# Kernel tuning notes

Hardware: AMD Instinct MI355X
Metric: run time of the kernel (lower is better)

The kernel has to match this reference:

```python
import jax, jax.numpy as jnp
import numpy as np

SCALE = 8.0  # sqrt(d_k=64)


def setup_inputs() -> dict:
    key = jax.random.key(0)
    kq, kk, kv, km = jax.random.split(key, 4)
    B, L, D = 8, 4096, 64
    q = jax.random.normal(kq, (B, L, D), dtype=jnp.float32)
    k = jax.random.normal(kk, (B, L, D), dtype=jnp.float32)
    v = jax.random.normal(kv, (B, L, D), dtype=jnp.float32)
    mask = jax.random.randint(km, (B, L, L), 0, 2) == 1  # True = masked out
    return {"q": q, "k": k, "v": v, "mask": mask}


def reference(q, k, v, mask):
    # scores: [B, Lq, Lk]
    u = jnp.einsum('bqd,bkd->bqk', q, k) / SCALE
    u = jnp.where(mask, -jnp.inf, u)
    attn = jax.nn.softmax(u, axis=2)
    output = jnp.einsum('bqk,bkd->bqd', attn, v)
    return (attn, output)
```

## Files before the change

### kernel.cpp

```cpp
#include <hip/hip_runtime.h>
#include <hip/hip_bf16.h>
#include <stdint.h>

#define BB 8
#define LL 4096
#define DD 64
#define KT 64
#define NT (LL / KT)
#define NP2 (LL / 128)

typedef short bf16x8 __attribute__((ext_vector_type(8)));
typedef float f32x4 __attribute__((ext_vector_type(4)));

#define QSCALE 0.1803368801111204f

__device__ inline short f2bfs(float x) {
    __hip_bfloat16 h = __float2bfloat16(x);
    return __builtin_bit_cast(short, h);
}

__device__ inline bf16x8 pack8v(f32x4 a, f32x4 b) {
    bf16x8 r;
    r[0] = f2bfs(a[0]); r[1] = f2bfs(a[1]); r[2] = f2bfs(a[2]); r[3] = f2bfs(a[3]);
    r[4] = f2bfs(b[0]); r[5] = f2bfs(b[1]); r[6] = f2bfs(b[2]); r[7] = f2bfs(b[3]);
    return r;
}

__device__ inline int swzK(int r) { return (r & 3) | (((r >> 3) & 1) << 2); }
__device__ inline int swzV(int r) { return (r & 7) ^ ((r >> 3) & 7); }

__device__ inline void wg_barrier() {
    asm volatile("s_waitcnt lgkmcnt(0)" ::: "memory");
    __builtin_amdgcn_s_barrier();
    __builtin_amdgcn_sched_barrier(0);
}

__device__ inline void gl_lds16(const ushort* g, ushort* l) {
    __builtin_amdgcn_global_load_lds((const __attribute__((address_space(1))) void*)g,
                                     (__attribute__((address_space(3))) void*)l, 16, 0, 0);
}

__global__ void detect_mask_kernel(const uint32_t* __restrict__ w, uint32_t* __restrict__ flag) {
    __shared__ int nonbin;
    if (threadIdx.x == 0) nonbin = 0;
    __syncthreads();
    int bad = 0;
    for (int i = threadIdx.x; i < 4096; i += 256) bad |= (w[i] > 1u) ? 1 : 0;
    if (bad) atomicOr(&nonbin, 1);
    __syncthreads();
    if (threadIdx.x == 0) *flag = (uint32_t)(nonbin != 0);
}

__global__ void convert_k_kernel(const float* __restrict__ src, ushort* __restrict__ dst) {
    const int i = blockIdx.x * 256 + threadIdx.x;
    f32x4 a = *(const f32x4*)(src + (size_t)i * 8);
    f32x4 b = *(const f32x4*)(src + (size_t)i * 8 + 4);
    *(bf16x8*)(dst + (size_t)i * 8) = pack8v(a, b);
}

__global__ void convert_vt_kernel(const float* __restrict__ v, ushort* __restrict__ vt) {
    __shared__ alignas(16) float Lt[64][68];
    const int kt = blockIdx.x, b = blockIdx.y;
    const int tid = (int)threadIdx.x;
    const int r = tid >> 2, c4 = tid & 3;
    const float* vb = v + ((size_t)b * LL + kt * 64) * DD;
    #pragma unroll
    for (int j = 0; j < 4; ++j)
        *(f32x4*)&Lt[r][c4 * 16 + j * 4] = *(const f32x4*)(vb + (size_t)r * DD + c4 * 16 + j * 4);
    __syncthreads();
    ushort* vout = vt + (size_t)b * DD * LL + (size_t)r * LL + kt * 64 + c4 * 16;
    bf16x8 o0, o1;
    #pragma unroll
    for (int j = 0; j < 8; ++j) o0[j] = f2bfs(Lt[c4 * 16 + j][r]);
    #pragma unroll
    for (int j = 0; j < 8; ++j) o1[j] = f2bfs(Lt[c4 * 16 + 8 + j][r]);
    *(bf16x8*)vout = o0;
    *(bf16x8*)(vout + 8) = o1;
}

__global__ __launch_bounds__(512, 4) void fused_attn_kernel(
    const float* __restrict__ qg, const ushort* __restrict__ kbf,
    const ushort* __restrict__ vtb, const void* __restrict__ maskv,
    const uint32_t* __restrict__ flagp,
    float* __restrict__ attn, float* __restrict__ outp)
{
    __shared__ alignas(16) ushort KB[4][KT * 64];
    __shared__ uint8_t Msk[8][NT][64];
    __shared__ float Rs[128];

    const int tid = (int)threadIdx.x;
    const int w   = tid >> 6, l = tid & 63;
    const int lr  = l & 15, lg = l >> 4;
    const int rg  = w & 3, ch = w >> 2;
    const int id  = (int)blockIdx.x;
    const int b   = id & 7;
    const int q0  = (id >> 3) * 64;
    const bool mbyte = (*flagp != 0);

    const ushort* kb = kbf + (size_t)b * LL * DD;
    const ushort* vtg = vtb + (size_t)b * DD * LL;

    const int qrow = q0 + 16 * rg + lr;
    const uint8_t* mrow8  = (const uint8_t*)maskv + (size_t)b * LL * LL + (size_t)qrow * LL + ch * 32 + lg * 8;
    const int*     mrow32 = (const int*)maskv     + (size_t)b * LL * LL + (size_t)qrow * LL + ch * 32 + lg * 8;
    float* arow = attn + (size_t)b * LL * LL + (size_t)qrow * LL + ch * 32 + lg * 8;

    bf16x8 qf0, qf1;
    {
        const float* qp = qg + (size_t)(b * LL + qrow) * DD + lg * 8;
        qf0 = pack8v(*(const f32x4*)(qp)      * QSCALE, *(const f32x4*)(qp + 4)  * QSCALE);
        qf1 = pack8v(*(const f32x4*)(qp + 32) * QSCALE, *(const f32x4*)(qp + 36) * QSCALE);
    }

    const int drow = w * 8 + (l >> 3);
    const int dc   = l & 7;
    const int kchunk = dc ^ swzK(drow);
    const int vchunk = dc ^ swzV(drow);
    auto dmaK = [&](int kt, int buf) {
        gl_lds16(kb + (size_t)(kt * KT + drow) * 64 + 8 * kchunk, &KB[buf][w * 512]);
    };
    auto dmaV = [&](int kt, int buf) {
        gl_lds16(vtg + (size_t)drow * LL + kt * KT + 8 * vchunk, &KB[2 + buf][w * 512]);
    };
    auto dmaK2 = [&](int kt2, int pair) {
        gl_lds16(kb + (size_t)(kt2 * 128 + drow) * 64 + 8 * kchunk, &KB[2 * pair][w * 512]);
        gl_lds16(kb + (size_t)(kt2 * 128 + 64 + drow) * 64 + 8 * kchunk, &KB[2 * pair + 1][w * 512]);
    };
    unsigned long long mA = 0, mB = 0;
    #define ASM_MLOAD(dst, kt) { unsigned long long a_ = (unsigned long long)(uintptr_t)(mrow8 + (kt) * KT); \
        asm volatile("global_load_dwordx2 %0, %1, off" : "=v"(dst) : "v"(a_) : "memory"); }

    float rsum = 0.f;
    f32x4 oacc[4];
    #pragma unroll
    for (int g = 0; g < 4; ++g) { f32x4 z = {0.f, 0.f, 0.f, 0.f}; oacc[g] = z; }

    auto body1 = [&](int buf, unsigned long long mu, int kt) {
        int4 mi0 = {0,0,0,0}, mi1 = {0,0,0,0};
        if (!mbyte) { mi0 = *(const int4*)(mrow32 + kt * KT); mi1 = *(const int4*)(mrow32 + kt * KT + 4); }
        uint32_t mbits = 0;
        float p8[8];
        __builtin_amdgcn_s_setprio(1);
        #pragma unroll
        for (int n = 0; n < 2; ++n) {
            const int krow = ch * 32 + ((lr >> 2) << 3) + (n << 2) + (lr & 3);
            bf16x8 k0 = *(const bf16x8*)&KB[buf][krow * 64 + ((lg       ^ swzK(krow)) << 3)];
            bf16x8 k1 = *(const bf16x8*)&KB[buf][krow * 64 + (((4 + lg) ^ swzK(krow)) << 3)];
            f32x4 c = {0.f, 0.f, 0.f, 0.f};
            c = __builtin_amdgcn_mfma_f32_16x16x32_bf16(k0, qf0, c, 0, 0, 0);
            c = __builtin_amdgcn_mfma_f32_16x16x32_bf16(k1, qf1, c, 0, 0, 0);
            #pragma unroll
            for (int j = 0; j < 4; ++j) {
                const int t = n * 4 + j;
                int mk;
                if (mbyte) mk = (int)((mu >> (8 * t)) & 0xffu);
                else {
                    const int4 mi = n ? mi1 : mi0;
                    mk = (j == 0) ? mi.x : (j == 1) ? mi.y : (j == 2) ? mi.z : mi.w;
                }
                mbits |= (mk ? 1u : 0u) << t;
                const float pv = mk ? 0.f : exp2f(c[j]);
                rsum += pv;
                p8[t] = pv;
            }
        }
        __builtin_amdgcn_s_setprio(0);
        Msk[w][kt][l] = (uint8_t)mbits;
        bf16x8 pa;
        #pragma unroll
        for (int t = 0; t < 8; ++t) pa[t] = f2bfs(p8[t]);
        __builtin_amdgcn_s_setprio(1);
        #pragma unroll
        for (int g = 0; g < 4; ++g) {
            const int d = g * 16 + lr;
            bf16x8 vf = *(const bf16x8*)&KB[2 + buf][d * 64 + (((ch * 4 + lg) ^ swzV(d)) << 3)];
            oacc[g] = __builtin_amdgcn_mfma_f32_16x16x32_bf16(pa, vf, oacc[g], 0, 0, 0);
        }
        __builtin_amdgcn_s_setprio(0);
    };

    dmaK(0, 0); dmaV(0, 0); if (mbyte) ASM_MLOAD(mA, 0);
    dmaK(1, 1); dmaV(1, 1); if (mbyte) ASM_MLOAD(mB, 1);
    #pragma unroll 1
    for (int kt = 0; kt < NT; kt += 2) {
        if (mbyte) asm volatile("s_waitcnt vmcnt(3)" ::: "memory");
        else       asm volatile("s_waitcnt vmcnt(2)" ::: "memory");
        __builtin_amdgcn_sched_barrier(0);
        wg_barrier();
        body1(0, mA, kt);
        wg_barrier();
        {
            const int nx = (kt + 2) & (NT - 1);
            dmaK(nx, 0); dmaV(nx, 0); if (mbyte) ASM_MLOAD(mA, nx);
        }
        if (mbyte) asm volatile("s_waitcnt vmcnt(3)" ::: "memory");
        else       asm volatile("s_waitcnt vmcnt(2)" ::: "memory");
        __builtin_amdgcn_sched_barrier(0);
        wg_barrier();
        body1(1, mB, kt + 1);
        wg_barrier();
        {
            const int nx = (kt + 3) & (NT - 1);
            dmaK(nx, 1); dmaV(nx, 1); if (mbyte) ASM_MLOAD(mB, nx);
        }
    }
    asm volatile("s_waitcnt vmcnt(0)" ::: "memory");

    rsum += __shfl_xor(rsum, 16, 64);
    rsum += __shfl_xor(rsum, 32, 64);
    if (lg == 0) Rs[ch * 64 + 16 * rg + lr] = rsum;
    __syncthreads();
    const float rinv = 1.0f / (Rs[16 * rg + lr] + Rs[64 + 16 * rg + lr]);

    float* OutL = (float*)KB;
    if (ch == 1) {
        #pragma unroll
        for (int g = 0; g < 4; ++g)
            #pragma unroll
            for (int j = 0; j < 4; ++j)
                OutL[rg * 1088 + (lg * 4 + j) * 68 + g * 16 + lr] = oacc[g][j];
    }
    __syncthreads();
    if (ch == 0) {
        #pragma unroll
        for (int j = 0; j < 4; ++j) {
            const int ql = 16 * rg + lg * 4 + j;
            const float ri = 1.0f / (Rs[ql] + Rs[64 + ql]);
            const size_t orow = (size_t)(b * LL + q0 + ql) * DD;
            #pragma unroll
            for (int g = 0; g < 4; ++g)
                outp[orow + g * 16 + lr] = (oacc[g][j] + OutL[rg * 1088 + (lg * 4 + j) * 68 + g * 16 + lr]) * ri;
        }
    }
    __syncthreads();

    auto body2 = [&](int pair, int idx) {
        const int kbase2 = idx * 128;
        #pragma unroll
        for (int h = 0; h < 2; ++h) {
            const int mb2 = (int)Msk[w][2 * idx + h][l];
            const ushort* Kbuf = KB[2 * pair + h];
            __builtin_amdgcn_s_setprio(1);
            #pragma unroll
            for (int n = 0; n < 2; ++n) {
                const int krow = ch * 32 + ((lr >> 2) << 3) + (n << 2) + (lr & 3);
                bf16x8 k0 = *(const bf16x8*)&Kbuf[krow * 64 + ((lg       ^ swzK(krow)) << 3)];
                bf16x8 k1 = *(const bf16x8*)&Kbuf[krow * 64 + (((4 + lg) ^ swzK(krow)) << 3)];
                f32x4 c = {0.f, 0.f, 0.f, 0.f};
                c = __builtin_amdgcn_mfma_f32_16x16x32_bf16(k0, qf0, c, 0, 0, 0);
                c = __builtin_amdgcn_mfma_f32_16x16x32_bf16(k1, qf1, c, 0, 0, 0);
                f32x4 pv;
                #pragma unroll
                for (int j = 0; j < 4; ++j)
                    pv[j] = ((mb2 >> (n * 4 + j)) & 1) ? 0.f : exp2f(c[j]) * rinv;
                *(f32x4*)(arow + kbase2 + h * 64 + n * 4) = pv;
            }
            __builtin_amdgcn_s_setprio(0);
        }
    };

    dmaK2(0, 0); dmaK2(1, 1);
    #pragma unroll 1
    for (int kt2 = 0; kt2 < NP2; ++kt2) {
        const int pair = kt2 & 1;
        asm volatile("s_waitcnt vmcnt(2)" ::: "memory");
        __builtin_amdgcn_sched_barrier(0);
        wg_barrier();
        body2(pair, kt2);
        wg_barrier();
        dmaK2((kt2 + 2) & (NP2 - 1), pair);
    }
    asm volatile("s_waitcnt vmcnt(0)" ::: "memory");
}

extern "C" void kernel_launch(void* const* d_in, const int* in_sizes, int n_in,
                              void* d_out, int out_size, void* d_ws, size_t ws_size,
                              hipStream_t stream) {
    const float* q = (const float*)d_in[0];
    const float* k = (const float*)d_in[1];
    const float* v = (const float*)d_in[2];
    const void* mask = d_in[3];
    float* attn = (float*)d_out;
    float* outp = attn + (size_t)BB * LL * LL;
    uint32_t* flagp = (uint32_t*)d_ws;
    ushort* kbf = (ushort*)((char*)d_ws + 4096);
    ushort* vtb = kbf + (size_t)BB * LL * DD;

    detect_mask_kernel<<<1, 256, 0, stream>>>((const uint32_t*)mask, flagp);
    convert_k_kernel<<<dim3(BB * LL * DD / 8 / 256), 256, 0, stream>>>(k, kbf);
    convert_vt_kernel<<<dim3(LL / 64, BB), 256, 0, stream>>>(v, vtb);
    fused_attn_kernel<<<dim3((LL / 64) * BB), 512, 0, stream>>>(q, kbf, vtb, mask, flagp, attn, outp);
}
```

Before: 364.3 us.

## Widen key tiles to 128 and reload mask in second pass instead of caching bits

Pass one now processes 128-key tiles, with each wave handling two 32-key subtiles and doing two P·V MFMAs per d-group, which halves the number of barriers and loop iterations. The LDS mask-bit cache is removed, and the second (attention-write) pass re-reads the mask from global memory alongside the K tiles. This cuts LDS usage and may allow more occupancy, at the cost of reading the mask twice from HBM and waiting on deeper vmcnt queues. The int-mask path now waits for vmcnt(0) every step.

```diff
diff --git a/kernel.cpp b/kernel.cpp
--- a/kernel.cpp
+++ b/kernel.cpp
@@ -5,9 +5,8 @@
 #define BB 8
 #define LL 4096
 #define DD 64
-#define KT 64
-#define NT (LL / KT)
-#define NP2 (LL / 128)
+#define KTW 128
+#define NTW (LL / KTW)
 
 typedef short bf16x8 __attribute__((ext_vector_type(8)));
 typedef float f32x4 __attribute__((ext_vector_type(4)));
@@ -84,8 +83,7 @@
     const uint32_t* __restrict__ flagp,
     float* __restrict__ attn, float* __restrict__ outp)
 {
-    __shared__ alignas(16) ushort KB[4][KT * 64];
-    __shared__ uint8_t Msk[8][NT][64];
+    __shared__ alignas(16) ushort KB[4][KTW * 64];
     __shared__ float Rs[128];
 
     const int tid = (int)threadIdx.x;
@@ -97,13 +95,13 @@
     const int q0  = (id >> 3) * 64;
     const bool mbyte = (*flagp != 0);
 
-    const ushort* kb = kbf + (size_t)b * LL * DD;
+    const ushort* kb  = kbf + (size_t)b * LL * DD;
     const ushort* vtg = vtb + (size_t)b * DD * LL;
 
     const int qrow = q0 + 16 * rg + lr;
-    const uint8_t* mrow8  = (const uint8_t*)maskv + (size_t)b * LL * LL + (size_t)qrow * LL + ch * 32 + lg * 8;
-    const int*     mrow32 = (const int*)maskv     + (size_t)b * LL * LL + (size_t)qrow * LL + ch * 32 + lg * 8;
-    float* arow = attn + (size_t)b * LL * LL + (size_t)qrow * LL + ch * 32 + lg * 8;
+    const uint8_t* mrow8  = (const uint8_t*)maskv + (size_t)b * LL * LL + (size_t)qrow * LL + ch * 64 + lg * 8;
+    const int*     mrow32 = (const int*)maskv     + (size_t)b * LL * LL + (size_t)qrow * LL + ch * 64 + lg * 8;
+    float* arow = attn + (size_t)b * LL * LL + (size_t)qrow * LL + ch * 64 + lg * 8;
 
     bf16x8 qf0, qf1;
     {
@@ -112,22 +110,21 @@
         qf1 = pack8v(*(const f32x4*)(qp + 32) * QSCALE, *(const f32x4*)(qp + 36) * QSCALE);
     }
 
-    const int drow = w * 8 + (l >> 3);
-    const int dc   = l & 7;
-    const int kchunk = dc ^ swzK(drow);
-    const int vchunk = dc ^ swzV(drow);
-    auto dmaK = [&](int kt, int buf) {
-        gl_lds16(kb + (size_t)(kt * KT + drow) * 64 + 8 * kchunk, &KB[buf][w * 512]);
-    };
-    auto dmaV = [&](int kt, int buf) {
-        gl_lds16(vtg + (size_t)drow * LL + kt * KT + 8 * vchunk, &KB[2 + buf][w * 512]);
-    };
-    auto dmaK2 = [&](int kt2, int pair) {
-        gl_lds16(kb + (size_t)(kt2 * 128 + drow) * 64 + 8 * kchunk, &KB[2 * pair][w * 512]);
-        gl_lds16(kb + (size_t)(kt2 * 128 + 64 + drow) * 64 + 8 * kchunk, &KB[2 * pair + 1][w * 512]);
-    };
-    unsigned long long mA = 0, mB = 0;
-    #define ASM_MLOAD(dst, kt) { unsigned long long a_ = (unsigned long long)(uintptr_t)(mrow8 + (kt) * KT); \
+    const int drK = w * 8 + (l >> 3), dcK = l & 7;
+    const int sK0 = dcK ^ swzK(drK);
+    const int dV  = l >> 4, cV = l & 15;
+
+    auto dmaK = [&](int kt, int slot) {
+        gl_lds16(kb + ((size_t)(kt * KTW + drK) << 6) + 8 * sK0,      &KB[slot][(w * 8) * 64]);
+        gl_lds16(kb + ((size_t)(kt * KTW + 64 + drK) << 6) + 8 * sK0, &KB[slot][(w * 8 + 64) * 64]);
+    };
+    auto dmaV = [&](int kt, int slot) {
+        const int d0 = w * 8 + dV, d1 = w * 8 + 4 + dV;
+        gl_lds16(vtg + (size_t)d0 * LL + kt * KTW + 8 * (cV ^ swzV(d0)), &KB[2 + slot][(w * 8) * 128]);
+        gl_lds16(vtg + (size_t)d1 * LL + kt * KTW + 8 * (cV ^ swzV(d1)), &KB[2 + slot][(w * 8 + 4) * 128]);
+    };
+    unsigned long long mA0 = 0, mA1 = 0, mB0 = 0, mB1 = 0;
+    #define MLOAD(dst, off) { unsigned long long a_ = (unsigned long long)(uintptr_t)(mrow8 + (off)); \
         asm volatile("global_load_dwordx2 %0, %1, off" : "=v"(dst) : "v"(a_) : "memory"); }
 
     float rsum = 0.f;
@@ -135,74 +132,66 @@
     #pragma unroll
     for (int g = 0; g < 4; ++g) { f32x4 z = {0.f, 0.f, 0.f, 0.f}; oacc[g] = z; }
 
-    auto body1 = [&](int buf, unsigned long long mu, int kt) {
-        int4 mi0 = {0,0,0,0}, mi1 = {0,0,0,0};
-        if (!mbyte) { mi0 = *(const int4*)(mrow32 + kt * KT); mi1 = *(const int4*)(mrow32 + kt * KT + 4); }
-        uint32_t mbits = 0;
-        float p8[8];
+    auto body1 = [&](int slot, unsigned long long mu0, unsigned long long mu1, int kt) {
+        bf16x8 pa0, pa1;
         __builtin_amdgcn_s_setprio(1);
         #pragma unroll
-        for (int n = 0; n < 2; ++n) {
-            const int krow = ch * 32 + ((lr >> 2) << 3) + (n << 2) + (lr & 3);
-            bf16x8 k0 = *(const bf16x8*)&KB[buf][krow * 64 + ((lg       ^ swzK(krow)) << 3)];
-            bf16x8 k1 = *(const bf16x8*)&KB[buf][krow * 64 + (((4 + lg) ^ swzK(krow)) << 3)];
-            f32x4 c = {0.f, 0.f, 0.f, 0.f};
-            c = __builtin_amdgcn_mfma_f32_16x16x32_bf16(k0, qf0, c, 0, 0, 0);
-            c = __builtin_amdgcn_mfma_f32_16x16x32_bf16(k1, qf1, c, 0, 0, 0);
-            #pragma unroll
-            for (int j = 0; j < 4; ++j) {
-                const int t = n * 4 + j;
-                int mk;
-                if (mbyte) mk = (int)((mu >> (8 * t)) & 0xffu);
-                else {
-                    const int4 mi = n ? mi1 : mi0;
-                    mk = (j == 0) ? mi.x : (j == 1) ? mi.y : (j == 2) ? mi.z : mi.w;
+        for (int s = 0; s < 2; ++s) {
+            #pragma unroll
+            for (int n = 0; n < 2; ++n) {
+                const int krow = ch * 64 + s * 32 + ((lr >> 2) << 3) + (n << 2) + (lr & 3);
+                bf16x8 k0 = *(const bf16x8*)&KB[slot][krow * 64 + ((lg       ^ swzK(krow)) << 3)];
+                bf16x8 k1 = *(const bf16x8*)&KB[slot][krow * 64 + (((4 + lg) ^ swzK(krow)) << 3)];
+                f32x4 c = {0.f, 0.f, 0.f, 0.f};
+                c = __builtin_amdgcn_mfma_f32_16x16x32_bf16(k0, qf0, c, 0, 0, 0);
+                c = __builtin_amdgcn_mfma_f32_16x16x32_bf16(k1, qf1, c, 0, 0, 0);
+                int4 mi = {0, 0, 0, 0};
+                if (!mbyte) mi = *(const int4*)(mrow32 + kt * KTW + s * 32 + n * 4);
+                #pragma unroll
+                for (int j = 0; j < 4; ++j) {
+                    const int t = n * 4 + j;
+                    int mk;
+                    if (mbyte) mk = (int)(((s ? mu1 : mu0) >> (8 * t)) & 0xffu);
+                    else       mk = (j == 0) ? mi.x : (j == 1) ? mi.y : (j == 2) ? mi.z : mi.w;
+                    const float pv = mk ? 0.f : exp2f(c[j]);
+                    rsum += pv;
+                    if (s) pa1[t] = f2bfs(pv); else pa0[t] = f2bfs(pv);
                 }
-                mbits |= (mk ? 1u : 0u) << t;
-                const float pv = mk ? 0.f : exp2f(c[j]);
-                rsum += pv;
-                p8[t] = pv;
             }
         }
-        __builtin_amdgcn_s_setprio(0);
-        Msk[w][kt][l] = (uint8_t)mbits;
-        bf16x8 pa;
-        #pragma unroll
-        for (int t = 0; t < 8; ++t) pa[t] = f2bfs(p8[t]);
-        __builtin_amdgcn_s_setprio(1);
         #pragma unroll
         for (int g = 0; g < 4; ++g) {
             const int d = g * 16 + lr;
-            bf16x8 vf = *(const bf16x8*)&KB[2 + buf][d * 64 + (((ch * 4 + lg) ^ swzV(d)) << 3)];
-            oacc[g] = __builtin_amdgcn_mfma_f32_16x16x32_bf16(pa, vf, oacc[g], 0, 0, 0);
+            bf16x8 vf0 = *(const bf16x8*)&KB[2 + slot][d * 128 + (((ch * 8 + lg)     ^ swzV(d)) << 3)];
+            oacc[g] = __builtin_amdgcn_mfma_f32_16x16x32_bf16(pa0, vf0, oacc[g], 0, 0, 0);
+            bf16x8 vf1 = *(const bf16x8*)&KB[2 + slot][d * 128 + (((ch * 8 + 4 + lg) ^ swzV(d)) << 3)];
+            oacc[g] = __builtin_amdgcn_mfma_f32_16x16x32_bf16(pa1, vf1, oacc[g], 0, 0, 0);
         }
         __builtin_amdgcn_s_setprio(0);
     };
 
-    dmaK(0, 0); dmaV(0, 0); if (mbyte) ASM_MLOAD(mA, 0);
-    dmaK(1, 1); dmaV(1, 1); if (mbyte) ASM_MLOAD(mB, 1);
+    dmaK(0, 0); dmaV(0, 0); if (mbyte) { MLOAD(mA0, 0); MLOAD(mA1, 32); }
+    dmaK(1, 1); dmaV(1, 1); if (mbyte) { MLOAD(mB0, KTW); MLOAD(mB1, KTW + 32); }
     #pragma unroll 1
-    for (int kt = 0; kt < NT; kt += 2) {
-        if (mbyte) asm volatile("s_waitcnt vmcnt(3)" ::: "memory");
-        else       asm volatile("s_waitcnt vmcnt(2)" ::: "memory");
-        __builtin_amdgcn_sched_barrier(0);
-        wg_barrier();
-        body1(0, mA, kt);
-        wg_barrier();
-        {
-            const int nx = (kt + 2) & (NT - 1);
-            dmaK(nx, 0); dmaV(nx, 0); if (mbyte) ASM_MLOAD(mA, nx);
-        }
-        if (mbyte) asm volatile("s_waitcnt vmcnt(3)" ::: "memory");
-        else       asm volatile("s_waitcnt vmcnt(2)" ::: "memory");
-        __builtin_amdgcn_sched_barrier(0);
-        wg_barrier();
-        body1(1, mB, kt + 1);
-        wg_barrier();
-        {
-            const int nx = (kt + 3) & (NT - 1);
-            dmaK(nx, 1); dmaV(nx, 1); if (mbyte) ASM_MLOAD(mB, nx);
-        }
+    for (int kt = 0; kt < NTW; kt += 2) {
+        if (mbyte) asm volatile("s_waitcnt vmcnt(6)" ::: "memory");
+        else       asm volatile("s_waitcnt vmcnt(0)" ::: "memory");
+        __builtin_amdgcn_sched_barrier(0);
+        wg_barrier();
+        body1(0, mA0, mA1, kt);
+        wg_barrier();
+        {   const int nx = (kt + 2) & (NTW - 1);
+            dmaK(nx, 0); dmaV(nx, 0);
+            if (mbyte) { MLOAD(mA0, nx * KTW); MLOAD(mA1, nx * KTW + 32); } }
+        if (mbyte) asm volatile("s_waitcnt vmcnt(6)" ::: "memory");
+        else       asm volatile("s_waitcnt vmcnt(0)" ::: "memory");
+        __builtin_amdgcn_sched_barrier(0);
+        wg_barrier();
+        body1(1, mB0, mB1, kt + 1);
+        wg_barrier();
+        {   const int nx = (kt + 3) & (NTW - 1);
+            dmaK(nx, 1); dmaV(nx, 1);
+            if (mbyte) { MLOAD(mB0, nx * KTW); MLOAD(mB1, nx * KTW + 32); } }
     }
     asm volatile("s_waitcnt vmcnt(0)" ::: "memory");
 
@@ -234,41 +223,57 @@
     }
     __syncthreads();
 
-    auto body2 = [&](int pair, int idx) {
-        const int kbase2 = idx * 128;
-        #pragma unroll
-        for (int h = 0; h < 2; ++h) {
-            const int mb2 = (int)Msk[w][2 * idx + h][l];
-            const ushort* Kbuf = KB[2 * pair + h];
-            __builtin_amdgcn_s_setprio(1);
+    auto body2 = [&](int slot, unsigned long long mu0, unsigned long long mu1, int kt) {
+        __builtin_amdgcn_s_setprio(1);
+        #pragma unroll
+        for (int s = 0; s < 2; ++s) {
             #pragma unroll
             for (int n = 0; n < 2; ++n) {
-                const int krow = ch * 32 + ((lr >> 2) << 3) + (n << 2) + (lr & 3);
-                bf16x8 k0 = *(const bf16x8*)&Kbuf[krow * 64 + ((lg       ^ swzK(krow)) << 3)];
-                bf16x8 k1 = *(const bf16x8*)&Kbuf[krow * 64 + (((4 + lg) ^ swzK(krow)) << 3)];
+                const int krow = ch * 64 + s * 32 + ((lr >> 2) << 3) + (n << 2) + (lr & 3);
+                bf16x8 k0 = *(const bf16x8*)&KB[slot][krow * 64 + ((lg       ^ swzK(krow)) << 3)];
+                bf16x8 k1 = *(const bf16x8*)&KB[slot][krow * 64 + (((4 + lg) ^ swzK(krow)) << 3)];
                 f32x4 c = {0.f, 0.f, 0.f, 0.f};
                 c = __builtin_amdgcn_mfma_f32_16x16x32_bf16(k0, qf0, c, 0, 0, 0);
                 c = __builtin_amdgcn_mfma_f32_16x16x32_bf16(k1, qf1, c, 0, 0, 0);
+                int4 mi = {0, 0, 0, 0};
+                if (!mbyte) mi = *(const int4*)(mrow32 + kt * KTW + s * 32 + n * 4);
                 f32x4 pv;
                 #pragma unroll
-                for (int j = 0; j < 4; ++j)
-                    pv[j] = ((mb2 >> (n * 4 + j)) & 1) ? 0.f : exp2f(c[j]) * rinv;
-                *(f32x4*)(arow + kbase2 + h * 64 + n * 4) = pv;
+                for (int j = 0; j < 4; ++j) {
+                    const int t = n * 4 + j;
+                    int mk;
+                    if (mbyte) mk = (int)(((s ? mu1 : mu0) >> (8 * t)) & 0xffu);
+                    else       mk = (j == 0) ? mi.x : (j == 1) ? mi.y : (j == 2) ? mi.z : mi.w;
+                    pv[j] = mk ? 0.f : exp2f(c[j]) * rinv;
+                }
+                *(f32x4*)(arow + kt * KTW + s * 32 + n * 4) = pv;
             }
-            __builtin_amdgcn_s_setprio(0);
-        }
-    };
-
-    dmaK2(0, 0); dmaK2(1, 1);
+        }
+        __builtin_amdgcn_s_setprio(0);
+    };
+
+    dmaK(0, 0); if (mbyte) { MLOAD(mA0, 0); MLOAD(mA1, 32); }
+    dmaK(1, 1); if (mbyte) { MLOAD(mB0, KTW); MLOAD(mB1, KTW + 32); }
     #pragma unroll 1
-    for (int kt2 = 0; kt2 < NP2; ++kt2) {
-        const int pair = kt2 & 1;
-        asm volatile("s_waitcnt vmcnt(2)" ::: "memory");
-        __builtin_amdgcn_sched_barrier(0);
-        wg_barrier();
-        body2(pair, kt2);
-        wg_barrier();
-        dmaK2((kt2 + 2) & (NP2 - 1), pair);
+    for (int kt = 0; kt < NTW; kt += 2) {
+        if (mbyte) asm volatile("s_waitcnt vmcnt(4)" ::: "memory");
+        else       asm volatile("s_waitcnt vmcnt(0)" ::: "memory");
+        __builtin_amdgcn_sched_barrier(0);
+        wg_barrier();
+        body2(0, mA0, mA1, kt);
+        wg_barrier();
+        {   const int nx = (kt + 2) & (NTW - 1);
+            dmaK(nx, 0);
+            if (mbyte) { MLOAD(mA0, nx * KTW); MLOAD(mA1, nx * KTW + 32); } }
+        if (mbyte) asm volatile("s_waitcnt vmcnt(4)" ::: "memory");
+        else       asm volatile("s_waitcnt vmcnt(0)" ::: "memory");
+        __builtin_amdgcn_sched_barrier(0);
+        wg_barrier();
+        body2(1, mB0, mB1, kt + 1);
+        wg_barrier();
+        {   const int nx = (kt + 3) & (NTW - 1);
+            dmaK(nx, 1);
+            if (mbyte) { MLOAD(mB0, nx * KTW); MLOAD(mB1, nx * KTW + 32); } }
     }
     asm volatile("s_waitcnt vmcnt(0)" ::: "memory");
 }
```

Result: slower. 488.3 us (+34.0%).
